# Kernel tuning notes

Measured on AMD Instinct MI355X. Metric: run time of the kernel, lower is better.

The kernel has to match this reference:

```python
import jax, jax.numpy as jnp
import numpy as np

NUM_EMBEDDINGS = 1024
EMBEDDING_DIM = 64
COMMITMENT_COST = 0.25


def setup_inputs() -> dict:
    key = jax.random.key(0)
    k1, k2 = jax.random.split(key)
    inputs = jax.random.normal(k1, (32, EMBEDDING_DIM, 64, 64), dtype=jnp.float32)
    # torch init: uniform(-1/K, 1/K)
    weight = jax.random.uniform(
        k2, (NUM_EMBEDDINGS, EMBEDDING_DIM), dtype=jnp.float32,
        minval=-1.0 / NUM_EMBEDDINGS, maxval=1.0 / NUM_EMBEDDINGS)
    return {"inputs": inputs, "weight": weight}


def reference(inputs, weight):
    # NCHW -> NHWC
    x = jnp.transpose(inputs, (0, 2, 3, 1))  # [B,H,W,D]
    B, H, W, D = x.shape
    flat = x.reshape(-1, D)  # [N,D]
    # squared L2 distances to each codebook entry: [N,K]
    distances = (
        jnp.sum(flat ** 2, axis=1, keepdims=True)
        + jnp.sum(weight ** 2, axis=1)
        - 2.0 * flat @ weight.T
    )
    encoding_indices = jnp.argmin(distances, axis=1)  # [N]
    # one-hot @ weight is just a gather
    quantized = weight[encoding_indices].reshape(x.shape)  # [B,H,W,D]

    e_latent_loss = jnp.mean((jax.lax.stop_gradient(quantized) - x) ** 2)
    q_latent_loss = jnp.mean((quantized - jax.lax.stop_gradient(x)) ** 2)
    loss = q_latent_loss + COMMITMENT_COST * e_latent_loss

    # straight-through estimator
    quantized_st = x + jax.lax.stop_gradient(quantized - x)
    out = jnp.transpose(quantized_st, (0, 3, 1, 2))  # NHWC -> NCHW
    return out, loss, encoding_indices[:, None]
```

## Files before the change

### kernel.cpp

```cpp
#include <hip/hip_runtime.h>
#include <math.h>

#define N_ROWS   131072
#define DIM      64
#define KCODES   1024
#define HWSZ     4096
#define CHW      262144
#define OUT_ELEMS 8388608
#define BLOCK    512
#define HALF_T   256
#define PIX      2
#define PIXBLK   (HALF_T * PIX)
#define NBLOCKS  (N_ROWS / PIXBLK)
#define KHALF    512
#define TILE_K   128

__device__ __forceinline__ float np_sumsq64(const float* v) {
#pragma clang fp contract(off)
    float r[8];
#pragma unroll
    for (int j = 0; j < 8; ++j) r[j] = v[j] * v[j];
#pragma unroll
    for (int i = 8; i < 64; i += 8) {
#pragma unroll
        for (int j = 0; j < 8; ++j) {
            float p = v[i + j] * v[i + j];
            r[j] = r[j] + p;
        }
    }
    float s01 = r[0] + r[1];
    float s23 = r[2] + r[3];
    float s45 = r[4] + r[5];
    float s67 = r[6] + r[7];
    return (s01 + s23) + (s45 + s67);
}

__global__ __launch_bounds__(256) void vq_wsum(const float* __restrict__ w,
                                               float* __restrict__ wsum) {
    int k = blockIdx.x * blockDim.x + threadIdx.x;
    const float* wr = w + k * DIM;
    float wv[DIM];
#pragma unroll
    for (int d = 0; d < DIM; ++d) wv[d] = wr[d];
    wsum[k] = np_sumsq64(wv);
}

__global__ __launch_bounds__(512, 1) void vq_main(const float* __restrict__ inp,
                                                  const float* __restrict__ weight,
                                                  const float* __restrict__ wsum,
                                                  float* __restrict__ out,
                                                  float* __restrict__ idx_out,
                                                  float* __restrict__ block_loss) {
    __shared__ float sw[2][TILE_K * DIM];
    __shared__ float sws[2][TILE_K];
    __shared__ float cbv[2][HALF_T];
    __shared__ int   cbk[2][HALF_T];
    __shared__ float red[BLOCK / 64];

    const int tid  = threadIdx.x;
    const int half = tid >> 8;
    const int t    = tid & 255;
    const int n0   = blockIdx.x * PIXBLK + t;
    const int n1   = n0 + HALF_T;
    const int b0 = n0 >> 12, hw0 = n0 & 4095;
    const int b1 = n1 >> 12, hw1 = n1 & 4095;

    const float* xb0 = inp + (size_t)b0 * CHW + hw0;
    const float* xb1 = inp + (size_t)b1 * CHW + hw1;
    float x0[DIM], x1[DIM];
#pragma unroll
    for (int d = 0; d < DIM; ++d) x0[d] = xb0[(size_t)d * HWSZ];
#pragma unroll
    for (int d = 0; d < DIM; ++d) x1[d] = xb1[(size_t)d * HWSZ];

    const float a0 = np_sumsq64(x0);
    const float a1 = np_sumsq64(x1);

    float best0 = 3.402823466e38f, best1 = 3.402823466e38f;
    int   bk0 = 0, bk1 = 0;

    const int kbase = half * KHALF;

    for (int tile = 0; tile < KHALF; tile += TILE_K) {
        __syncthreads();
        {
            const float4* gsrc = (const float4*)(weight + (size_t)(kbase + tile) * DIM);
            float4* ldst = (float4*)sw[half];
#pragma unroll
            for (int i = 0; i < 8; ++i)
                ldst[i * HALF_T + t] = gsrc[i * HALF_T + t];
            if (t < TILE_K) sws[half][t] = wsum[kbase + tile + t];
        }
        __syncthreads();

        for (int kk = 0; kk < TILE_K; kk += 2) {
            const float* wp0 = &sw[half][kk * DIM];
            const float* wp1 = wp0 + DIM;
            float c00 = 0.f, c01 = 0.f, c10 = 0.f, c11 = 0.f;
#pragma unroll
            for (int d = 0; d < DIM; ++d) {
                const float wa = wp0[d];
                const float wb = wp1[d];
                c00 = __builtin_fmaf(x0[d], wa, c00);
                c10 = __builtin_fmaf(x1[d], wa, c10);
                c01 = __builtin_fmaf(x0[d], wb, c01);
                c11 = __builtin_fmaf(x1[d], wb, c11);
            }
            float dk00, dk01, dk10, dk11;
            {
#pragma clang fp contract(off)
                const float sa = a0 + sws[half][kk];
                const float sb = a0 + sws[half][kk + 1];
                const float ta = a1 + sws[half][kk];
                const float tb = a1 + sws[half][kk + 1];
                dk00 = sa - 2.0f * c00;
                dk01 = sb - 2.0f * c01;
                dk10 = ta - 2.0f * c10;
                dk11 = tb - 2.0f * c11;
            }
            const int k0 = kbase + tile + kk;
            if (dk00 < best0) { best0 = dk00; bk0 = k0; }
            if (dk01 < best0) { best0 = dk01; bk0 = k0 + 1; }
            if (dk10 < best1) { best1 = dk10; bk1 = k0; }
            if (dk11 < best1) { best1 = dk11; bk1 = k0 + 1; }
        }
    }

    __syncthreads();
    if (half == 0) {
        cbv[0][t] = best0; cbk[0][t] = bk0;
        cbv[1][t] = best1; cbk[1][t] = bk1;
    }
    __syncthreads();

    float ls = 0.f;
    if (half == 1) {
        const float lo0 = cbv[0][t]; const int lk0 = cbk[0][t];
        const float lo1 = cbv[1][t]; const int lk1 = cbk[1][t];
        if (!(best0 < lo0)) { best0 = lo0; bk0 = lk0; }
        if (!(best1 < lo1)) { best1 = lo1; bk1 = lk1; }

        const float* wb0 = weight + bk0 * DIM;
        const float* wb1 = weight + bk1 * DIM;
        float* ob0 = out + (size_t)b0 * CHW + hw0;
        float* ob1 = out + (size_t)b1 * CHW + hw1;
#pragma unroll
        for (int c = 0; c < DIM; ++c) {
            const float wv0 = wb0[c];
            ob0[(size_t)c * HWSZ] = wv0;
            const float d0 = wv0 - x0[c];
            ls = fmaf(d0, d0, ls);
            const float wv1 = wb1[c];
            ob1[(size_t)c * HWSZ] = wv1;
            const float d1 = wv1 - x1[c];
            ls = fmaf(d1, d1, ls);
        }
        idx_out[n0] = (float)bk0;
        idx_out[n1] = (float)bk1;
    }

#pragma unroll
    for (int off = 32; off > 0; off >>= 1) ls += __shfl_down(ls, off, 64);
    const int lane = tid & 63;
    const int wid  = tid >> 6;
    if (lane == 0) red[wid] = ls;
    __syncthreads();
    if (tid == 0) {
        float s = 0.f;
#pragma unroll
        for (int w = 0; w < BLOCK / 64; ++w) s += red[w];
        block_loss[blockIdx.x] = s;
    }
}

__global__ __launch_bounds__(256) void vq_loss_reduce(const float* __restrict__ bl,
                                                      float* __restrict__ loss_out) {
    double s = 0.0;
    for (int i = threadIdx.x; i < NBLOCKS; i += 256) s += (double)bl[i];
    __shared__ double red[4];
#pragma unroll
    for (int off = 32; off > 0; off >>= 1) s += __shfl_down(s, off, 64);
    const int lane = threadIdx.x & 63;
    const int wid  = threadIdx.x >> 6;
    if (lane == 0) red[wid] = s;
    __syncthreads();
    if (threadIdx.x == 0) {
        const double total = (red[0] + red[1]) + (red[2] + red[3]);
        loss_out[0] = (float)(1.25 * total / (double)OUT_ELEMS);
    }
}

extern "C" void kernel_launch(void* const* d_in, const int* in_sizes, int n_in,
                              void* d_out, int out_size, void* d_ws, size_t ws_size,
                              hipStream_t stream) {
    const float* inp    = (const float*)d_in[0];
    const float* weight = (const float*)d_in[1];

    float* out_q    = (float*)d_out;
    float* out_loss = (float*)d_out + OUT_ELEMS;
    float* out_idx  = (float*)d_out + OUT_ELEMS + 1;

    float* wsum       = (float*)d_ws;
    float* block_loss = (float*)d_ws + KCODES;

    vq_wsum<<<KCODES / 256, 256, 0, stream>>>(weight, wsum);
    vq_main<<<NBLOCKS, BLOCK, 0, stream>>>(inp, weight, wsum,
                                           out_q, out_idx, block_loss);
    vq_loss_reduce<<<1, BLOCK / 2, 0, stream>>>(block_loss, out_loss);
}
```

Measured before the change: 331.2 us.

## Software-pipeline codebook LDS reads with float4 register double-buffering and larger tiles

The inner distance loop is restructured so codebook rows are read from shared memory as float4 into two alternating register buffers, with the next quarter-row prefetched while the current one feeds the FMAs. The codebook tile grows from 128 to 256 codes, padded by two rows so the prefetch past the last pair stays in bounds. Launch bounds are raised to request two blocks per CU. This aims to hide LDS latency and halve tile-load barriers, but it roughly doubles shared memory per block and caps registers on top of the 128 already holding the two pixels, which risks spills and may leave the requested occupancy out of reach.

```diff
diff --git a/kernel.cpp b/kernel.cpp
--- a/kernel.cpp
+++ b/kernel.cpp
@@ -13,7 +13,8 @@
 #define PIXBLK   (HALF_T * PIX)
 #define NBLOCKS  (N_ROWS / PIXBLK)
 #define KHALF    512
-#define TILE_K   128
+#define TILE_K   256
+#define TILE_PAD (TILE_K + 2)
 
 __device__ __forceinline__ float np_sumsq64(const float* v) {
 #pragma clang fp contract(off)
@@ -45,13 +46,44 @@
     wsum[k] = np_sumsq64(wv);
 }
 
-__global__ __launch_bounds__(512, 1) void vq_main(const float* __restrict__ inp,
+__device__ __forceinline__ void loadq(const float4* __restrict__ swv,
+                                      int kka, int kkb, int q,
+                                      float4 (&r0)[4], float4 (&r1)[4]) {
+#pragma unroll
+    for (int j = 0; j < 4; ++j) {
+        r0[j] = swv[kka * 16 + q * 4 + j];
+        r1[j] = swv[kkb * 16 + q * 4 + j];
+    }
+}
+
+__device__ __forceinline__ void fma16(const float4 (&r0)[4], const float4 (&r1)[4],
+                                      const float* __restrict__ x0,
+                                      const float* __restrict__ x1, int db,
+                                      float& c00, float& c01,
+                                      float& c10, float& c11) {
+#pragma unroll
+    for (int j = 0; j < 4; ++j) {
+        const float4 va = r0[j];
+        const float4 vb = r1[j];
+        const int d = db + j * 4;
+        c00 = __builtin_fmaf(x0[d + 0], va.x, c00); c10 = __builtin_fmaf(x1[d + 0], va.x, c10);
+        c01 = __builtin_fmaf(x0[d + 0], vb.x, c01); c11 = __builtin_fmaf(x1[d + 0], vb.x, c11);
+        c00 = __builtin_fmaf(x0[d + 1], va.y, c00); c10 = __builtin_fmaf(x1[d + 1], va.y, c10);
+        c01 = __builtin_fmaf(x0[d + 1], vb.y, c01); c11 = __builtin_fmaf(x1[d + 1], vb.y, c11);
+        c00 = __builtin_fmaf(x0[d + 2], va.z, c00); c10 = __builtin_fmaf(x1[d + 2], va.z, c10);
+        c01 = __builtin_fmaf(x0[d + 2], vb.z, c01); c11 = __builtin_fmaf(x1[d + 2], vb.z, c11);
+        c00 = __builtin_fmaf(x0[d + 3], va.w, c00); c10 = __builtin_fmaf(x1[d + 3], va.w, c10);
+        c01 = __builtin_fmaf(x0[d + 3], vb.w, c01); c11 = __builtin_fmaf(x1[d + 3], vb.w, c11);
+    }
+}
+
+__global__ __launch_bounds__(512, 2) void vq_main(const float* __restrict__ inp,
                                                   const float* __restrict__ weight,
                                                   const float* __restrict__ wsum,
                                                   float* __restrict__ out,
                                                   float* __restrict__ idx_out,
                                                   float* __restrict__ block_loss) {
-    __shared__ float sw[2][TILE_K * DIM];
+    __shared__ float sw[2][TILE_PAD * DIM];
     __shared__ float sws[2][TILE_K];
     __shared__ float cbv[2][HALF_T];
     __shared__ int   cbk[2][HALF_T];
@@ -80,39 +112,45 @@
     int   bk0 = 0, bk1 = 0;
 
     const int kbase = half * KHALF;
+    const float4* swv = (const float4*)(&sw[half][0]);
 
     for (int tile = 0; tile < KHALF; tile += TILE_K) {
         __syncthreads();
         {
             const float4* gsrc = (const float4*)(weight + (size_t)(kbase + tile) * DIM);
-            float4* ldst = (float4*)sw[half];
-#pragma unroll
-            for (int i = 0; i < 8; ++i)
+            float4* ldst = (float4*)(&sw[half][0]);
+#pragma unroll
+            for (int i = 0; i < 16; ++i)
                 ldst[i * HALF_T + t] = gsrc[i * HALF_T + t];
-            if (t < TILE_K) sws[half][t] = wsum[kbase + tile + t];
+            sws[half][t] = wsum[kbase + tile + t];
         }
         __syncthreads();
 
+        float4 A0[4], A1[4], B0[4], B1[4];
+        loadq(swv, 0, 1, 0, A0, A1);
+
+#pragma unroll 1
         for (int kk = 0; kk < TILE_K; kk += 2) {
-            const float* wp0 = &sw[half][kk * DIM];
-            const float* wp1 = wp0 + DIM;
+            const float bsw0 = sws[half][kk];
+            const float bsw1 = sws[half][kk + 1];
             float c00 = 0.f, c01 = 0.f, c10 = 0.f, c11 = 0.f;
-#pragma unroll
-            for (int d = 0; d < DIM; ++d) {
-                const float wa = wp0[d];
-                const float wb = wp1[d];
-                c00 = __builtin_fmaf(x0[d], wa, c00);
-                c10 = __builtin_fmaf(x1[d], wa, c10);
-                c01 = __builtin_fmaf(x0[d], wb, c01);
-                c11 = __builtin_fmaf(x1[d], wb, c11);
-            }
+
+            loadq(swv, kk, kk + 1, 1, B0, B1);
+            fma16(A0, A1, x0, x1, 0,  c00, c01, c10, c11);
+            loadq(swv, kk, kk + 1, 2, A0, A1);
+            fma16(B0, B1, x0, x1, 16, c00, c01, c10, c11);
+            loadq(swv, kk, kk + 1, 3, B0, B1);
+            fma16(A0, A1, x0, x1, 32, c00, c01, c10, c11);
+            loadq(swv, kk + 2, kk + 3, 0, A0, A1);
+            fma16(B0, B1, x0, x1, 48, c00, c01, c10, c11);
+
             float dk00, dk01, dk10, dk11;
             {
 #pragma clang fp contract(off)
-                const float sa = a0 + sws[half][kk];
-                const float sb = a0 + sws[half][kk + 1];
-                const float ta = a1 + sws[half][kk];
-                const float tb = a1 + sws[half][kk + 1];
+                const float sa = a0 + bsw0;
+                const float sb = a0 + bsw1;
+                const float ta = a1 + bsw0;
+                const float tb = a1 + bsw1;
                 dk00 = sa - 2.0f * c00;
                 dk01 = sb - 2.0f * c01;
                 dk10 = ta - 2.0f * c10;
```

After: 313.6 us. 1.06x faster.

## Replace LDS weight tiles with wave-uniform scalar loads and packed FMA

Applied to the files above, without the earlier changes.

Removes the shared-memory staging of codebook tiles and the per-tile barriers. Each wave instead reads codebook rows straight from global memory through a wave-uniform (readfirstlane) pointer, so the loads can become scalar loads, and the next row is software-prefetched into registers. The two pixels per thread are packed into 2-wide vectors so the dot products can map to packed FMA instructions. Occupancy hint is raised to 2 blocks per CU. The risks are scalar-load latency and register pressure from keeping 128 pixel values plus 64 weight values live, which could limit occupancy.

```diff
diff --git a/kernel.cpp b/kernel.cpp
--- a/kernel.cpp
+++ b/kernel.cpp
@@ -13,7 +13,20 @@
 #define PIXBLK   (HALF_T * PIX)
 #define NBLOCKS  (N_ROWS / PIXBLK)
 #define KHALF    512
-#define TILE_K   128
+
+typedef float v2f __attribute__((ext_vector_type(2)));
+
+__device__ __forceinline__ v2f fma2(v2f a, float b, v2f c) {
+#if __has_builtin(__builtin_elementwise_fma)
+    v2f bb = {b, b};
+    return __builtin_elementwise_fma(a, bb, c);
+#else
+    v2f r;
+    r[0] = __builtin_fmaf(a[0], b, c[0]);
+    r[1] = __builtin_fmaf(a[1], b, c[1]);
+    return r;
+#endif
+}
 
 __device__ __forceinline__ float np_sumsq64(const float* v) {
 #pragma clang fp contract(off)
@@ -35,6 +48,30 @@
     return (s01 + s23) + (s45 + s67);
 }
 
+__device__ __forceinline__ float np_sumsq64_s2(const float* v, int off) {
+#pragma clang fp contract(off)
+    float r[8];
+#pragma unroll
+    for (int j = 0; j < 8; ++j) {
+        const float t = v[2 * j + off];
+        r[j] = t * t;
+    }
+#pragma unroll
+    for (int i = 8; i < 64; i += 8) {
+#pragma unroll
+        for (int j = 0; j < 8; ++j) {
+            const float t = v[2 * (i + j) + off];
+            const float p = t * t;
+            r[j] = r[j] + p;
+        }
+    }
+    float s01 = r[0] + r[1];
+    float s23 = r[2] + r[3];
+    float s45 = r[4] + r[5];
+    float s67 = r[6] + r[7];
+    return (s01 + s23) + (s45 + s67);
+}
+
 __global__ __launch_bounds__(256) void vq_wsum(const float* __restrict__ w,
                                                float* __restrict__ wsum) {
     int k = blockIdx.x * blockDim.x + threadIdx.x;
@@ -45,20 +82,18 @@
     wsum[k] = np_sumsq64(wv);
 }
 
-__global__ __launch_bounds__(512, 1) void vq_main(const float* __restrict__ inp,
+__global__ __launch_bounds__(512, 2) void vq_main(const float* __restrict__ inp,
                                                   const float* __restrict__ weight,
                                                   const float* __restrict__ wsum,
                                                   float* __restrict__ out,
                                                   float* __restrict__ idx_out,
                                                   float* __restrict__ block_loss) {
-    __shared__ float sw[2][TILE_K * DIM];
-    __shared__ float sws[2][TILE_K];
     __shared__ float cbv[2][HALF_T];
     __shared__ int   cbk[2][HALF_T];
     __shared__ float red[BLOCK / 64];
 
     const int tid  = threadIdx.x;
-    const int half = tid >> 8;
+    const int half = __builtin_amdgcn_readfirstlane(tid >> 8);
     const int t    = tid & 255;
     const int n0   = blockIdx.x * PIXBLK + t;
     const int n1   = n0 + HALF_T;
@@ -67,63 +102,60 @@
 
     const float* xb0 = inp + (size_t)b0 * CHW + hw0;
     const float* xb1 = inp + (size_t)b1 * CHW + hw1;
-    float x0[DIM], x1[DIM];
-#pragma unroll
-    for (int d = 0; d < DIM; ++d) x0[d] = xb0[(size_t)d * HWSZ];
-#pragma unroll
-    for (int d = 0; d < DIM; ++d) x1[d] = xb1[(size_t)d * HWSZ];
-
-    const float a0 = np_sumsq64(x0);
-    const float a1 = np_sumsq64(x1);
+    v2f xp[DIM];
+#pragma unroll
+    for (int d = 0; d < DIM; ++d) {
+        v2f v;
+        v[0] = xb0[(size_t)d * HWSZ];
+        v[1] = xb1[(size_t)d * HWSZ];
+        xp[d] = v;
+    }
+
+    const float a0 = np_sumsq64_s2((const float*)xp, 0);
+    const float a1 = np_sumsq64_s2((const float*)xp, 1);
 
     float best0 = 3.402823466e38f, best1 = 3.402823466e38f;
     int   bk0 = 0, bk1 = 0;
 
     const int kbase = half * KHALF;
-
-    for (int tile = 0; tile < KHALF; tile += TILE_K) {
-        __syncthreads();
+    const float* __restrict__ wb = weight + (size_t)kbase * DIM;
+    const float* __restrict__ ws = wsum + kbase;
+
+    float wA[32], wB[32];
+#pragma unroll
+    for (int j = 0; j < 32; ++j) wA[j] = wb[j];
+
+#pragma unroll 1
+    for (int k = 0; k < KHALF; ++k) {
+        const float bsw = ws[k];
+        const int   kn  = (k + 1 < KHALF) ? (k + 1) : 0;
+        const float* rk  = wb + k * DIM;
+        const float* rkn = wb + kn * DIM;
+
+#pragma unroll
+        for (int j = 0; j < 32; ++j) wB[j] = rk[32 + j];
+
+        v2f c = {0.f, 0.f};
+#pragma unroll
+        for (int j = 0; j < 32; ++j) c = fma2(xp[j], wA[j], c);
+
+#pragma unroll
+        for (int j = 0; j < 32; ++j) wA[j] = rkn[j];
+
+#pragma unroll
+        for (int j = 0; j < 32; ++j) c = fma2(xp[32 + j], wB[j], c);
+
+        float dk0, dk1;
         {
-            const float4* gsrc = (const float4*)(weight + (size_t)(kbase + tile) * DIM);
-            float4* ldst = (float4*)sw[half];
-#pragma unroll
-            for (int i = 0; i < 8; ++i)
-                ldst[i * HALF_T + t] = gsrc[i * HALF_T + t];
-            if (t < TILE_K) sws[half][t] = wsum[kbase + tile + t];
-        }
-        __syncthreads();
-
-        for (int kk = 0; kk < TILE_K; kk += 2) {
-            const float* wp0 = &sw[half][kk * DIM];
-            const float* wp1 = wp0 + DIM;
-            float c00 = 0.f, c01 = 0.f, c10 = 0.f, c11 = 0.f;
-#pragma unroll
-            for (int d = 0; d < DIM; ++d) {
-                const float wa = wp0[d];
-                const float wb = wp1[d];
-                c00 = __builtin_fmaf(x0[d], wa, c00);
-                c10 = __builtin_fmaf(x1[d], wa, c10);
-                c01 = __builtin_fmaf(x0[d], wb, c01);
-                c11 = __builtin_fmaf(x1[d], wb, c11);
-            }
-            float dk00, dk01, dk10, dk11;
-            {
 #pragma clang fp contract(off)
-                const float sa = a0 + sws[half][kk];
-                const float sb = a0 + sws[half][kk + 1];
-                const float ta = a1 + sws[half][kk];
-                const float tb = a1 + sws[half][kk + 1];
-                dk00 = sa - 2.0f * c00;
-                dk01 = sb - 2.0f * c01;
-                dk10 = ta - 2.0f * c10;
-                dk11 = tb - 2.0f * c11;
-            }
-            const int k0 = kbase + tile + kk;
-            if (dk00 < best0) { best0 = dk00; bk0 = k0; }
-            if (dk01 < best0) { best0 = dk01; bk0 = k0 + 1; }
-            if (dk10 < best1) { best1 = dk10; bk1 = k0; }
-            if (dk11 < best1) { best1 = dk11; bk1 = k0 + 1; }
-        }
+            const float sa = a0 + bsw;
+            const float ta = a1 + bsw;
+            dk0 = sa - 2.0f * c[0];
+            dk1 = ta - 2.0f * c[1];
+        }
+        const int kg = kbase + k;
+        if (dk0 < best0) { best0 = dk0; bk0 = kg; }
+        if (dk1 < best1) { best1 = dk1; bk1 = kg; }
     }
 
     __syncthreads();
@@ -148,11 +180,11 @@
         for (int c = 0; c < DIM; ++c) {
             const float wv0 = wb0[c];
             ob0[(size_t)c * HWSZ] = wv0;
-            const float d0 = wv0 - x0[c];
+            const float d0 = wv0 - xp[c][0];
             ls = fmaf(d0, d0, ls);
             const float wv1 = wb1[c];
             ob1[(size_t)c * HWSZ] = wv1;
-            const float d1 = wv1 - x1[c];
+            const float d1 = wv1 - xp[c][1];
             ls = fmaf(d1, d1, ls);
         }
         idx_out[n0] = (float)bk0;
```

Result: slower. 422.1 us (+27.5%).
